# Kernel tuning notes

Hardware: AMD Instinct MI355X
Metric: run time of the kernel (lower is better)

The kernel has to match this reference:

```python
import jax, jax.numpy as jnp
import numpy as np

VOCAB = 100000
EMBED = 256
HIDDEN = 512
H = HIDDEN // 2          # per-direction LSTM hidden
K = 12                   # tagset size
START = 10
STOP = 11
B = 64
T = 512
NEG = -10000.0


def setup_inputs() -> dict:
    key = jax.random.key(0)
    ks = jax.random.split(key, 14)
    s = 1.0 / np.sqrt(H)
    u = lambda k, shape: jax.random.uniform(k, shape, jnp.float32, -s, s)
    transitions = jax.random.normal(ks[12], (K, K), jnp.float32)
    transitions = transitions.at[START, :].set(NEG).at[:, STOP].set(NEG)
    return {
        "sentence": jax.random.randint(ks[0], (B, T), 0, VOCAB),
        "sentence_len": jnp.full((B,), T, dtype=jnp.int32),
        "embed_table": jax.random.normal(ks[1], (VOCAB, EMBED), jnp.float32),
        "Wf_ih": u(ks[2], (4 * H, EMBED)),
        "Wf_hh": u(ks[3], (4 * H, H)),
        "bf_ih": u(ks[4], (4 * H,)),
        "bf_hh": u(ks[5], (4 * H,)),
        "Wb_ih": u(ks[6], (4 * H, EMBED)),
        "Wb_hh": u(ks[7], (4 * H, H)),
        "bb_ih": u(ks[8], (4 * H,)),
        "bb_hh": u(ks[9], (4 * H,)),
        "W_out": u(ks[10], (K, HIDDEN)),
        "b_out": u(ks[11], (K,)),
        "transitions": transitions,
    }


def _lstm_scan(x_proj, W_hh, reverse):
    # x_proj: [T, B, 4H] (input projection + both biases already added)
    def step(carry, xt):
        h, c = carry
        g = xt + h @ W_hh.T
        i, f, gg, o = jnp.split(g, 4, axis=-1)  # torch gate order i,f,g,o
        i = jax.nn.sigmoid(i)
        f = jax.nn.sigmoid(f)
        gg = jnp.tanh(gg)
        o = jax.nn.sigmoid(o)
        c = f * c + i * gg
        h = o * jnp.tanh(c)
        return (h, c), h

    h0 = jnp.zeros((x_proj.shape[1], W_hh.shape[1]), x_proj.dtype)
    _, hs = jax.lax.scan(step, (h0, h0), x_proj, reverse=reverse)
    return hs  # [T, B, H]


def reference(sentence, sentence_len, embed_table,
              Wf_ih, Wf_hh, bf_ih, bf_hh,
              Wb_ih, Wb_hh, bb_ih, bb_hh,
              W_out, b_out, transitions):
    emb = embed_table[sentence]                                   # [B,T,E]
    xf = (jnp.einsum('bte,ge->btg', emb, Wf_ih) + bf_ih + bf_hh).transpose(1, 0, 2)
    xb = (jnp.einsum('bte,ge->btg', emb, Wb_ih) + bb_ih + bb_hh).transpose(1, 0, 2)
    hf = _lstm_scan(xf, Wf_hh, reverse=False)                     # [T,B,H]
    hb = _lstm_scan(xb, Wb_hh, reverse=True)                      # [T,B,H]
    hcat = jnp.concatenate([hf, hb], axis=-1)                     # [T,B,2H]
    feats = jnp.einsum('tbh,kh->tbk', hcat, W_out) + b_out        # [T,B,K]

    nb = sentence.shape[0]
    nt = feats.shape[0]
    kt = transitions.shape[0]
    dp0 = jnp.full((nb, kt), NEG, feats.dtype).at[:, START].set(0.0)
    mask = jnp.arange(nt)[:, None] < sentence_len[None, :]        # [T,B]
    ident = jnp.arange(kt)[None, :]

    def vstep(dp, inp):
        ft, mt = inp                                              # [B,K], [B]
        scores = dp[:, None, :] + transitions[None, :, :]         # [B,Knext,Kprev]
        bptr = jnp.argmax(scores, axis=2)
        dp_new = jnp.max(scores, axis=2) + ft
        dp = jnp.where(mt[:, None], dp_new, dp)
        bptr = jnp.where(mt[:, None], bptr, ident)
        return dp, bptr

    dp, bptrs = jax.lax.scan(vstep, dp0, (feats, mask))           # bptrs: [T,B,K]
    terminal = dp + transitions[STOP][None, :]
    best_last = jnp.argmax(terminal, axis=1)                      # [B]
    path_scores = jnp.max(terminal, axis=1)                       # [B]

    def bstep(tag, bp):
        prev = jnp.take_along_axis(bp, tag[:, None], axis=1)[:, 0]
        return prev, tag

    _, path = jax.lax.scan(bstep, best_last, bptrs, reverse=True)  # [T,B]
    return path_scores, path.transpose(1, 0)
```

## Files before the change

kernel.cpp:

```cpp
#include <hip/hip_runtime.h>
#include <math.h>

#define BATCH 64
#define TLEN 512
#define EMB 256
#define HID 256
#define G4 1024
#define KTAG 12
#define START_TAG 10
#define STOP_TAG 11
#define NEGV -10000.0f
#define SENT 0xFFFFFFFFu

#define LOG2E 1.4426950408889634f

typedef float f4 __attribute__((ext_vector_type(4)));

__device__ __forceinline__ float fsig(float x) {
    return __builtin_amdgcn_rcpf(1.f + __builtin_amdgcn_exp2f(-LOG2E * x));
}
__device__ __forceinline__ float ftanh(float x) {
    return 1.f - 2.f * __builtin_amdgcn_rcpf(1.f + __builtin_amdgcn_exp2f(2.f * LOG2E * x));
}
__device__ __forceinline__ void st_llc(float* p, float v) {
    __hip_atomic_store(p, v, __ATOMIC_RELAXED, __HIP_MEMORY_SCOPE_AGENT);
}
__device__ __forceinline__ unsigned ld_llc_u(const unsigned* p) {
    return __hip_atomic_load(p, __ATOMIC_RELAXED, __HIP_MEMORY_SCOPE_AGENT);
}

#define MT 128
#define NT 128
#define KC 32
#define LDP 132

__global__ __launch_bounds__(256) void proj_kernel(
    const int* __restrict__ sentence, const float* __restrict__ emb,
    const float* __restrict__ Wf_ih, const float* __restrict__ Wb_ih,
    const float* __restrict__ bf_ih, const float* __restrict__ bf_hh,
    const float* __restrict__ bb_ih, const float* __restrict__ bb_hh,
    float* __restrict__ xf, float* __restrict__ xb) {
    int mtile = blockIdx.x;
    int ntile = blockIdx.y;
    int tid = threadIdx.x;

    __shared__ float As[KC][LDP];
    __shared__ float Bs[KC][LDP];
    __shared__ int tok[MT];

    int g2base = ntile * NT;
    const bool fwd = (g2base < 1024);
    const float* Wih = fwd ? Wf_ih : Wb_ih;
    const float* bia = fwd ? bf_ih : bb_ih;
    const float* bib = fwd ? bf_hh : bb_hh;
    float* dst       = fwd ? xf    : xb;
    int glb = g2base & 1023;

    if (tid < MT) tok[tid] = sentence[(size_t)mtile * MT + tid];
    __syncthreads();

    float acc[8][8];
#pragma unroll
    for (int i = 0; i < 8; ++i)
#pragma unroll
        for (int jj = 0; jj < 8; ++jj) acc[i][jj] = 0.f;

    int m0 = (tid & 15) * 8;
    int n0 = (tid >> 4) * 8;
    int lr = tid >> 3;
    int lk = (tid & 7) * 4;

    for (int k0 = 0; k0 < EMB; k0 += KC) {
#pragma unroll
        for (int i = 0; i < 4; ++i) {
            int r = lr + 32 * i;
            float4 v = *(const float4*)(emb + (size_t)tok[r] * EMB + k0 + lk);
            As[lk + 0][r] = v.x; As[lk + 1][r] = v.y;
            As[lk + 2][r] = v.z; As[lk + 3][r] = v.w;
            float4 w = *(const float4*)(Wih + (size_t)(glb + r) * EMB + k0 + lk);
            Bs[lk + 0][r] = w.x; Bs[lk + 1][r] = w.y;
            Bs[lk + 2][r] = w.z; Bs[lk + 3][r] = w.w;
        }
        __syncthreads();
#pragma unroll
        for (int kk = 0; kk < KC; ++kk) {
            float4 a0 = *(const float4*)&As[kk][m0];
            float4 a1 = *(const float4*)&As[kk][m0 + 4];
            float4 b0 = *(const float4*)&Bs[kk][n0];
            float4 b1 = *(const float4*)&Bs[kk][n0 + 4];
            float av[8] = {a0.x, a0.y, a0.z, a0.w, a1.x, a1.y, a1.z, a1.w};
            float bv[8] = {b0.x, b0.y, b0.z, b0.w, b1.x, b1.y, b1.z, b1.w};
#pragma unroll
            for (int i = 0; i < 8; ++i)
#pragma unroll
                for (int jj = 0; jj < 8; ++jj) acc[i][jj] += av[i] * bv[jj];
        }
        __syncthreads();
    }

    float bs[8];
#pragma unroll
    for (int jj = 0; jj < 8; ++jj) {
        int gl = glb + n0 + jj;
        bs[jj] = bia[gl] + bib[gl];
    }
#pragma unroll
    for (int i = 0; i < 8; ++i) {
        size_t r = (size_t)mtile * MT + m0 + i;
        float4 s0 = {acc[i][0] + bs[0], acc[i][1] + bs[1],
                     acc[i][2] + bs[2], acc[i][3] + bs[3]};
        float4 s1 = {acc[i][4] + bs[4], acc[i][5] + bs[5],
                     acc[i][6] + bs[6], acc[i][7] + bs[7]};
        *(float4*)(dst + r * (size_t)G4 + glb + n0)     = s0;
        *(float4*)(dst + r * (size_t)G4 + glb + n0 + 4) = s1;
    }
}

__global__ __launch_bounds__(256, 1) void lstm_scan10(
    const float* __restrict__ xf, const float* __restrict__ xb,
    const float* __restrict__ Wf_hh, const float* __restrict__ Wb_hh,
    float* __restrict__ hcat) {
    int blk = blockIdx.x;
    int grp = blk & 31;
    int s   = blk >> 5;
    int d   = grp >> 4;
    int gq  = grp & 15;
    int b0  = gq * 4;
    int tid = threadIdx.x;
    int kseg = tid & 7;
    int j    = tid >> 3;
    int J    = s * 32 + j;
    int bown = kseg & 3;

    __shared__ f4 Wl[4][8][256];
    __shared__ float hsL[2][4 * 288];

    const float* Whh = d ? Wb_hh : Wf_hh;
#pragma unroll
    for (int g = 0; g < 4; ++g)
#pragma unroll
        for (int q = 0; q < 8; ++q)
            Wl[g][q][tid] =
                *(const f4*)(Whh + (size_t)(g * 256 + J) * 256 + kseg * 32 + q * 4);

    f4 Wreg[4][4];
#pragma unroll
    for (int g = 0; g < 4; ++g)
#pragma unroll
        for (int q = 0; q < 4; ++q)
            Wreg[g][q] = Wl[g][q][tid];

    const float* x = d ? xb : xf;
    const float* xrow0 = x + (size_t)(b0 + bown) * TLEN * G4 + J;
    int sw = (tid >> 5) * 36 + (tid & 31);
    float c = 0.f;

    const float* xr0 = xrow0 + (size_t)(d ? (TLEN - 1) : 0) * G4;
    float xc0 = xr0[0], xc1 = xr0[256], xc2 = xr0[512], xc3 = xr0[768];

    for (int i = 0; i < TLEN; ++i) {
        int t = d ? (TLEN - 1 - i) : i;
        int buf = i & 1;

        if (i == 0) {
#pragma unroll
            for (int bb = 0; bb < 4; ++bb) hsL[0][bb * 288 + sw] = 0.f;
        } else {
            int tp = d ? (t + 1) : (t - 1);
            const unsigned* base = (const unsigned*)hcat +
                ((size_t)tp * BATCH + b0) * 512 + (size_t)d * HID + tid;
            unsigned u0, u1, u2, u3;
            for (;;) {
                u0 = ld_llc_u(base);
                u1 = ld_llc_u(base + 512);
                u2 = ld_llc_u(base + 1024);
                u3 = ld_llc_u(base + 1536);
                if (u0 != SENT && u1 != SENT && u2 != SENT && u3 != SENT) break;
                __builtin_amdgcn_s_sleep(1);
            }
            hsL[buf][0 * 288 + sw] = __uint_as_float(u0);
            hsL[buf][1 * 288 + sw] = __uint_as_float(u1);
            hsL[buf][2 * 288 + sw] = __uint_as_float(u2);
            hsL[buf][3 * 288 + sw] = __uint_as_float(u3);
        }
        __syncthreads();

        int tn = (i == TLEN - 1) ? t : (d ? (t - 1) : (t + 1));
        const float* xrn = xrow0 + (size_t)tn * G4;
        float xn0 = xrn[0], xn1 = xrn[256], xn2 = xrn[512], xn3 = xrn[768];

        float a[4][4];
#pragma unroll
        for (int g = 0; g < 4; ++g)
#pragma unroll
            for (int bb = 0; bb < 4; ++bb) a[g][bb] = 0.f;

        const float* hbase = hsL[buf] + kseg * 36;
#pragma unroll
        for (int q = 0; q < 8; ++q) {
            f4 w0, w1, w2, w3;
            if (q < 4) {
                w0 = Wreg[0][q]; w1 = Wreg[1][q];
                w2 = Wreg[2][q]; w3 = Wreg[3][q];
            } else {
                w0 = Wl[0][q][tid]; w1 = Wl[1][q][tid];
                w2 = Wl[2][q][tid]; w3 = Wl[3][q][tid];
            }
#pragma unroll
            for (int bb = 0; bb < 4; ++bb) {
                f4 h4 = *(const f4*)(hbase + bb * 288 + q * 4);
                a[0][bb] += w0.x*h4.x + w0.y*h4.y + w0.z*h4.z + w0.w*h4.w;
                a[1][bb] += w1.x*h4.x + w1.y*h4.y + w1.z*h4.z + w1.w*h4.w;
                a[2][bb] += w2.x*h4.x + w2.y*h4.y + w2.z*h4.z + w2.w*h4.w;
                a[3][bb] += w3.x*h4.x + w3.y*h4.y + w3.z*h4.z + w3.w*h4.w;
            }
        }

#pragma unroll
        for (int bb = 0; bb < 4; ++bb)
#pragma unroll
            for (int m = 1; m <= 4; m <<= 1) {
                a[0][bb] += __shfl_xor(a[0][bb], m);
                a[1][bb] += __shfl_xor(a[1][bb], m);
                a[2][bb] += __shfl_xor(a[2][bb], m);
                a[3][bb] += __shfl_xor(a[3][bb], m);
            }

        float A0 = bown == 0 ? a[0][0] : bown == 1 ? a[0][1] : bown == 2 ? a[0][2] : a[0][3];
        float A1 = bown == 0 ? a[1][0] : bown == 1 ? a[1][1] : bown == 2 ? a[1][2] : a[1][3];
        float A2 = bown == 0 ? a[2][0] : bown == 1 ? a[2][1] : bown == 2 ? a[2][2] : a[2][3];
        float A3 = bown == 0 ? a[3][0] : bown == 1 ? a[3][1] : bown == 2 ? a[3][2] : a[3][3];

        float ig = fsig(A0 + xc0);
        float fg = fsig(A1 + xc1);
        float gg = ftanh(A2 + xc2);
        float og = fsig(A3 + xc3);
        c = fg * c + ig * gg;
        float h = og * ftanh(c);
        if (kseg < 4)
            st_llc(hcat + ((size_t)t * BATCH + b0 + bown) * 512
                        + (size_t)d * HID + J, h);

        xc0 = xn0; xc1 = xn1; xc2 = xn2; xc3 = xn3;
    }
}

__global__ __launch_bounds__(256) void feats_kernel(
    const float* __restrict__ hcat, const float* __restrict__ Wout,
    const float* __restrict__ bout, float* __restrict__ feats) {
    int wid = threadIdx.x >> 6;
    int lane = threadIdx.x & 63;
    size_t row = (size_t)blockIdx.x * 4 + wid;
    const float* hrow = hcat + row * 512;
    float4 h0 = *(const float4*)(hrow + lane * 8);
    float4 h1 = *(const float4*)(hrow + lane * 8 + 4);
    for (int k2 = 0; k2 < KTAG; ++k2) {
        const float* wr = Wout + (size_t)k2 * 512 + lane * 8;
        float4 w0 = *(const float4*)wr;
        float4 w1 = *(const float4*)(wr + 4);
        float p = h0.x * w0.x + h0.y * w0.y + h0.z * w0.z + h0.w * w0.w
                + h1.x * w1.x + h1.y * w1.y + h1.z * w1.z + h1.w * w1.w;
#pragma unroll
        for (int off = 32; off; off >>= 1) p += __shfl_down(p, off);
        if (lane == 0) feats[row * KTAG + k2] = p + bout[k2];
    }
}

__global__ __launch_bounds__(64) void viterbi_kernel(
    const float* __restrict__ feats, const float* __restrict__ trans,
    const int* __restrict__ slen, float* __restrict__ out) {
    int b = blockIdx.x;
    int lane = threadIdx.x;
    __shared__ unsigned char bp[TLEN][KTAG];

    int len = slen[b];
    float tr[KTAG];
#pragma unroll
    for (int p = 0; p < KTAG; ++p) tr[p] = 0.f;
    if (lane < KTAG) {
#pragma unroll
        for (int p = 0; p < KTAG; ++p) tr[p] = trans[lane * KTAG + p];
    }
    float tstop = (lane < KTAG) ? trans[STOP_TAG * KTAG + lane] : NEGV;
    float dp = (lane == START_TAG) ? 0.f : NEGV;

    float fb[8];
#pragma unroll
    for (int k = 0; k < 8; ++k)
        fb[k] = (lane < KTAG) ? feats[((size_t)k * BATCH + b) * KTAG + lane] : 0.f;

    for (int t0 = 0; t0 < TLEN; t0 += 8) {
#pragma unroll
        for (int u = 0; u < 8; ++u) {
            int t = t0 + u;
            float ftc = fb[u];
            int tn = t + 8;
            fb[u] = (tn < TLEN && lane < KTAG)
                        ? feats[((size_t)tn * BATCH + b) * KTAG + lane] : 0.f;
            float best = -1e30f;
            int arg = 0;
#pragma unroll
            for (int p = 0; p < KTAG; ++p) {
                float dpp = __shfl(dp, p);
                float sc = dpp + tr[p];
                if (sc > best) { best = sc; arg = p; }
            }
            bool m = (t < len);
            if (lane < KTAG) {
                dp = m ? (best + ftc) : dp;
                bp[t][lane] = (unsigned char)(m ? arg : lane);
            }
        }
    }

    float term = dp + tstop;
    float bbest = -1e30f;
    int barg = 0;
#pragma unroll
    for (int p = 0; p < KTAG; ++p) {
        float v = __shfl(term, p);
        if (v > bbest) { bbest = v; barg = p; }
    }
    if (lane == 0) {
        out[b] = bbest;
        float* path = out + BATCH + (size_t)b * TLEN;
        int tag = barg;
        for (int t = TLEN - 1; t >= 0; --t) {
            path[t] = (float)tag;
            tag = bp[t][tag];
        }
    }
}

extern "C" void kernel_launch(void* const* d_in, const int* in_sizes, int n_in,
                              void* d_out, int out_size, void* d_ws, size_t ws_size,
                              hipStream_t stream) {
    const int*   sentence = (const int*)d_in[0];
    const int*   slen     = (const int*)d_in[1];
    const float* emb      = (const float*)d_in[2];
    const float* Wf_ih    = (const float*)d_in[3];
    const float* Wf_hh    = (const float*)d_in[4];
    const float* bf_ih    = (const float*)d_in[5];
    const float* bf_hh    = (const float*)d_in[6];
    const float* Wb_ih    = (const float*)d_in[7];
    const float* Wb_hh    = (const float*)d_in[8];
    const float* bb_ih    = (const float*)d_in[9];
    const float* bb_hh    = (const float*)d_in[10];
    const float* W_out    = (const float*)d_in[11];
    const float* b_out    = (const float*)d_in[12];
    const float* trans    = (const float*)d_in[13];
    float* out = (float*)d_out;

    char* ws = (char*)d_ws;
    float* xf    = (float*)(ws);
    float* xb    = (float*)(ws + 134217728ull);
    float* hcat  = (float*)(ws + 268435456ull);
    float* feats = (float*)(ws + 335544320ull);

    hipMemsetAsync(hcat, 0xFF, 67108864ull, stream);
    hipLaunchKernelGGL(proj_kernel, dim3(256, 16), dim3(256), 0, stream,
                       sentence, emb, Wf_ih, Wb_ih, bf_ih, bf_hh, bb_ih, bb_hh, xf, xb);
    hipLaunchKernelGGL(lstm_scan10, dim3(256), dim3(256), 0, stream,
                       xf, xb, Wf_hh, Wb_hh, hcat);
    hipLaunchKernelGGL(feats_kernel, dim3(8192), dim3(256), 0, stream,
                       hcat, W_out, b_out, feats);
    hipLaunchKernelGGL(viterbi_kernel, dim3(64), dim3(64), 0, stream,
                       feats, trans, slen, out);
}
```

Measured before the change: 2.297 ms.

## Give each wave a private copy of h state to drop block barriers

Each wavefront now loads the full previous hidden-state slice for its 4 batch rows into its own shared-memory region, 4 floats per lane. The per-step __syncthreads becomes a wave barrier, and the double buffer is no longer needed. This removes block-wide synchronisation from the serial recurrence. In exchange every wave polls and loads the hidden state redundantly, 16 L2 loads per lane instead of 4, so there is more global traffic and spin polling per step. It also relies on reads and writes to the single shared buffer being ordered within a wave.

```diff
diff --git a/kernel.cpp b/kernel.cpp
--- a/kernel.cpp
+++ b/kernel.cpp
@@ -116,7 +116,7 @@
     }
 }
 
-__global__ __launch_bounds__(256, 1) void lstm_scan10(
+__global__ __launch_bounds__(256, 1) void lstm_scan11(
     const float* __restrict__ xf, const float* __restrict__ xb,
     const float* __restrict__ Wf_hh, const float* __restrict__ Wb_hh,
     float* __restrict__ hcat) {
@@ -131,9 +131,11 @@
     int j    = tid >> 3;
     int J    = s * 32 + j;
     int bown = kseg & 3;
+    int wv   = tid >> 6;
+    int lane = tid & 63;
 
     __shared__ f4 Wl[4][8][256];
-    __shared__ float hsL[2][4 * 288];
+    __shared__ float hsL[4 * 1152];
 
     const float* Whh = d ? Wb_hh : Wf_hh;
 #pragma unroll
@@ -152,7 +154,9 @@
 
     const float* x = d ? xb : xf;
     const float* xrow0 = x + (size_t)(b0 + bown) * TLEN * G4 + J;
-    int sw = (tid >> 5) * 36 + (tid & 31);
+
+    float* hsW = hsL + wv * 1152;
+    int wsw = (lane >> 3) * 36 + (lane & 7) * 4;
     float c = 0.f;
 
     const float* xr0 = xrow0 + (size_t)(d ? (TLEN - 1) : 0) * G4;
@@ -160,30 +164,40 @@
 
     for (int i = 0; i < TLEN; ++i) {
         int t = d ? (TLEN - 1 - i) : i;
-        int buf = i & 1;
 
         if (i == 0) {
-#pragma unroll
-            for (int bb = 0; bb < 4; ++bb) hsL[0][bb * 288 + sw] = 0.f;
+            f4 z = {0.f, 0.f, 0.f, 0.f};
+#pragma unroll
+            for (int bb = 0; bb < 4; ++bb)
+                *(f4*)(hsW + bb * 288 + wsw) = z;
         } else {
             int tp = d ? (t + 1) : (t - 1);
             const unsigned* base = (const unsigned*)hcat +
-                ((size_t)tp * BATCH + b0) * 512 + (size_t)d * HID + tid;
-            unsigned u0, u1, u2, u3;
+                ((size_t)tp * BATCH + b0) * 512 + (size_t)d * HID + lane * 4;
+            unsigned u[16];
             for (;;) {
-                u0 = ld_llc_u(base);
-                u1 = ld_llc_u(base + 512);
-                u2 = ld_llc_u(base + 1024);
-                u3 = ld_llc_u(base + 1536);
-                if (u0 != SENT && u1 != SENT && u2 != SENT && u3 != SENT) break;
+#pragma unroll
+                for (int bb = 0; bb < 4; ++bb) {
+#pragma unroll
+                    for (int e = 0; e < 4; ++e)
+                        u[bb * 4 + e] = ld_llc_u(base + bb * 512 + e);
+                }
+                bool ok = true;
+#pragma unroll
+                for (int k = 0; k < 16; ++k) ok &= (u[k] != SENT);
+                if (ok) break;
                 __builtin_amdgcn_s_sleep(1);
             }
-            hsL[buf][0 * 288 + sw] = __uint_as_float(u0);
-            hsL[buf][1 * 288 + sw] = __uint_as_float(u1);
-            hsL[buf][2 * 288 + sw] = __uint_as_float(u2);
-            hsL[buf][3 * 288 + sw] = __uint_as_float(u3);
-        }
-        __syncthreads();
+#pragma unroll
+            for (int bb = 0; bb < 4; ++bb) {
+                f4 hv = {__uint_as_float(u[bb * 4 + 0]),
+                         __uint_as_float(u[bb * 4 + 1]),
+                         __uint_as_float(u[bb * 4 + 2]),
+                         __uint_as_float(u[bb * 4 + 3])};
+                *(f4*)(hsW + bb * 288 + wsw) = hv;
+            }
+        }
+        __builtin_amdgcn_wave_barrier();
 
         int tn = (i == TLEN - 1) ? t : (d ? (t - 1) : (t + 1));
         const float* xrn = xrow0 + (size_t)tn * G4;
@@ -195,7 +209,7 @@
 #pragma unroll
             for (int bb = 0; bb < 4; ++bb) a[g][bb] = 0.f;
 
-        const float* hbase = hsL[buf] + kseg * 36;
+        const float* hbase = hsW + kseg * 36;
 #pragma unroll
         for (int q = 0; q < 8; ++q) {
             f4 w0, w1, w2, w3;
@@ -360,7 +374,7 @@
     hipMemsetAsync(hcat, 0xFF, 67108864ull, stream);
     hipLaunchKernelGGL(proj_kernel, dim3(256, 16), dim3(256), 0, stream,
                        sentence, emb, Wf_ih, Wb_ih, bf_ih, bf_hh, bb_ih, bb_hh, xf, xb);
-    hipLaunchKernelGGL(lstm_scan10, dim3(256), dim3(256), 0, stream,
+    hipLaunchKernelGGL(lstm_scan11, dim3(256), dim3(256), 0, stream,
                        xf, xb, Wf_hh, Wb_hh, hcat);
     hipLaunchKernelGGL(feats_kernel, dim3(8192), dim3(256), 0, stream,
                        hcat, W_out, b_out, feats);
```

Measured after the change: 3.920 ms. +70.6%, slower.
